# Optimization experiments

Measured on AMD Instinct MI355X. Metric: run time of the kernel, lower is better.

The kernel has to match this reference:

```python
import jax, jax.numpy as jnp
import numpy as np

G = 4          # deformable groups (from offset_and_mask_dim = 3*4*3*3)
K = 9          # 3x3 kernel points
GN_GROUPS = 16 # GroupNorm groups as in DyHead


def conv2d(x, w, stride=1, pad=1, groups=1):
    return jax.lax.conv_general_dilated(
        x, w, (stride, stride), [(pad, pad), (pad, pad)],
        dimension_numbers=('NCHW', 'OIHW', 'NCHW'),
        feature_group_count=groups)


def dw_conv(x, w, scale, bias):
    # YOLO Conv with g=in_channels: depthwise 3x3 + folded BN + SiLU
    C = x.shape[1]
    y = conv2d(x, w, groups=C)
    y = y * scale[None, :, None, None] + bias[None, :, None, None]
    return y * jax.nn.sigmoid(y)


def offset_mask_conv(x, w, b):
    # Conv2d(C, 108, 3, padding=1, groups=4)
    return conv2d(x, w, groups=G) + b[None, :, None, None]


def split_offset_mask(om, use_softmax):
    # om: (N,108,H,W) -> offset (N,H,W,G,K,2) in pixels (dy,dx), mask (N,H,W,G,K)
    N, _, H, W = om.shape
    om = om.transpose(0, 2, 3, 1)
    offset = om[..., :2 * G * K].reshape(N, H, W, G, K, 2)
    m = om[..., 2 * G * K:].reshape(N, H, W, G, K)
    mask = jax.nn.softmax(m, axis=-1) if use_softmax else jax.nn.sigmoid(m)
    return offset, mask


def group_norm(x, gamma, beta, eps=1e-5):
    N, C, H, W = x.shape
    xg = x.reshape(N, GN_GROUPS, C // GN_GROUPS, H, W)
    mu = xg.mean((2, 3, 4), keepdims=True)
    var = xg.var((2, 3, 4), keepdims=True)
    xg = (xg - mu) * jax.lax.rsqrt(var + eps)
    return xg.reshape(N, C, H, W) * gamma[None, :, None, None] + beta[None, :, None, None]


def dcnv3_sample(x, offset, mask, stride):
    # DCNv3 core: group-wise deformable 3x3 bilinear sampling, zero padding.
    # x: (N,C,H,W); offset: (N,Ho,Wo,G,K,2); mask: (N,Ho,Wo,G,K) -> (N,C,Ho,Wo)
    N, C, H, W = x.shape
    Cg = C // G
    Ho, Wo = offset.shape[1], offset.shape[2]
    xg = x.transpose(0, 2, 3, 1).reshape(N, H, W, G, Cg)
    kk = jnp.arange(3, dtype=x.dtype) - 1.0
    ky = jnp.repeat(kk, 3)  # (9,)
    kx = jnp.tile(kk, 3)
    base_y = (jnp.arange(Ho, dtype=x.dtype) * stride)[None, :, None, None, None]
    base_x = (jnp.arange(Wo, dtype=x.dtype) * stride)[None, None, :, None, None]
    py = base_y + ky + offset[..., 0]   # (N,Ho,Wo,G,K)
    px = base_x + kx + offset[..., 1]
    y0 = jnp.floor(py)
    x0 = jnp.floor(px)
    wy = py - y0
    wx = px - x0
    y0i = y0.astype(jnp.int32)
    x0i = x0.astype(jnp.int32)
    n_idx = jnp.arange(N)[:, None, None, None, None]
    g_idx = jnp.arange(G)[None, None, None, :, None]
    acc = jnp.zeros((N, Ho, Wo, G, Cg), x.dtype)
    for dy in (0, 1):
        for dx in (0, 1):
            yi = y0i + dy
            xi = x0i + dx
            w = (wy if dy else 1.0 - wy) * (wx if dx else 1.0 - wx)
            valid = (yi >= 0) & (yi < H) & (xi >= 0) & (xi < W)
            w = w * valid.astype(x.dtype) * mask
            v = xg[n_idx, jnp.clip(yi, 0, H - 1), jnp.clip(xi, 0, W - 1), g_idx]  # (N,Ho,Wo,G,K,Cg)
            acc = acc + jnp.einsum('nhwgk,nhwgkc->nhwgc', w, v)
    return acc.reshape(N, Ho, Wo, C).transpose(0, 3, 1, 2)


def up_bilinear_ac(x, Ho, Wo):
    # bilinear, align_corners=True
    N, C, H, W = x.shape
    def coords(out, size):
        c = jnp.arange(out, dtype=jnp.float32) * ((size - 1) / max(out - 1, 1))
        i0 = jnp.floor(c).astype(jnp.int32)
        i1 = jnp.minimum(i0 + 1, size - 1)
        return i0, i1, (c - i0).astype(x.dtype)
    y0, y1, wy = coords(Ho, H)
    xc0, xc1, wx = coords(Wo, W)
    t = x[:, :, y0, :] * (1.0 - wy)[None, None, :, None] + x[:, :, y1, :] * wy[None, None, :, None]
    return t[:, :, :, xc0] * (1.0 - wx) + t[:, :, :, xc1] * wx


def scale_attn(f, w, b):
    # AdaptiveAvgPool2d(1) -> Conv 1x1 (C->1) -> ReLU -> HSigmoid(bias=3, divisor=6)
    y = f.mean((2, 3))                      # (N,C)
    a = jax.nn.relu(y @ w.T + b)            # (N,1)
    a = jnp.clip((a + 3.0) / 6.0, 0.0, 1.0)
    return f * a[:, :, None, None]


def dyrelu(f, w1, b1_, w2, b2_):
    # DyReLU with K2=True, use_bias=True, lambda_a=2, init_a=[1,0], init_b=[0,0]
    y = f.mean((2, 3))                      # (N,C)
    h = jax.nn.relu(y @ w1.T + b1_)
    z = jnp.clip(h @ w2.T + b2_ + 3.0, 0.0, 6.0) / 6.0  # h_sigmoid
    a1, b1, a2, b2 = jnp.split(z, 4, axis=1)
    a1 = (a1 - 0.5) * 2.0 + 1.0
    a2 = (a2 - 0.5) * 2.0
    b1 = b1 - 0.5
    b2 = b2 - 0.5
    bc = lambda t: t[:, :, None, None]
    return jnp.maximum(f * bc(a1) + bc(b1), f * bc(a2) + bc(b2))


def _forward(x0, x1, x2,
             dw_w_h, dw_s_h, dw_b_h, dw_w_m, dw_s_m, dw_b_m, dw_w_l, dw_s_l, dw_b_l,
             off_w, off_b,
             gn_g_h, gn_b_h, gn_g_m, gn_b_m, gn_g_l, gn_b_l,
             sa_w, sa_b, fc1_w, fc1_b, fc2_w, fc2_b):
    xs = [x0, x1, x2]
    outs = []
    for lvl in range(3):
        x = xs[lvl]
        mid_ = dw_conv(x, dw_w_m, dw_s_m, dw_b_m)
        off, msk = split_offset_mask(offset_mask_conv(mid_, off_w, off_b), use_softmax=False)
        mid_feat = group_norm(dcnv3_sample(x, off, msk, 1), gn_g_m, gn_b_m)
        sum_feat = scale_attn(mid_feat, sa_w, sa_b)
        n_lvls = 1
        if lvl > 0:
            xl = xs[lvl - 1]
            low_ = dw_conv(xl, dw_w_l, dw_s_l, dw_b_l)
            off, msk = split_offset_mask(offset_mask_conv(low_, off_w, off_b), use_softmax=True)
            off = off[:, ::2, ::2]   # stride-2 output grid
            msk = msk[:, ::2, ::2]
            low_feat = group_norm(dcnv3_sample(xl, off, msk, 2), gn_g_l, gn_b_l)
            sum_feat = sum_feat + scale_attn(low_feat, sa_w, sa_b)
            n_lvls += 1
        if lvl < 2:
            xh = xs[lvl + 1]
            high_ = dw_conv(xh, dw_w_h, dw_s_h, dw_b_h)
            off, msk = split_offset_mask(offset_mask_conv(high_, off_w, off_b), use_softmax=True)
            high_feat = group_norm(dcnv3_sample(xh, off, msk, 1), gn_g_h, gn_b_h)
            high_feat = up_bilinear_ac(high_feat, x.shape[2], x.shape[3])
            sum_feat = sum_feat + scale_attn(high_feat, sa_w, sa_b)
            n_lvls += 1
        outs.append(dyrelu(sum_feat / n_lvls, fc1_w, fc1_b, fc2_w, fc2_b))
    return tuple(outs)


def setup_inputs() -> dict:
    key = jax.random.key(0)
    ks = jax.random.split(key, 32)
    N, C = 4, 256
    f32 = jnp.float32
    nrm = lambda k, shape, s=1.0: jax.random.normal(k, shape, f32) * s
    inp = {
        'x0': nrm(ks[0], (N, C, 80, 80)),
        'x1': nrm(ks[1], (N, C, 40, 40)),
        'x2': nrm(ks[2], (N, C, 20, 20)),
        'dw_w_h': nrm(ks[3], (C, 1, 3, 3), 0.1),
        'dw_s_h': 1.0 + nrm(ks[4], (C,), 0.1),
        'dw_b_h': nrm(ks[5], (C,), 0.1),
        'dw_w_m': nrm(ks[6], (C, 1, 3, 3), 0.1),
        'dw_s_m': 1.0 + nrm(ks[7], (C,), 0.1),
        'dw_b_m': nrm(ks[8], (C,), 0.1),
        'dw_w_l': nrm(ks[9], (C, 1, 3, 3), 0.1),
        'dw_s_l': 1.0 + nrm(ks[10], (C,), 0.1),
        'dw_b_l': nrm(ks[11], (C,), 0.1),
        'off_w': nrm(ks[12], (108, C // G, 3, 3), 0.1),
        'off_b': nrm(ks[13], (108,), 0.1),
        'gn_g_h': 1.0 + nrm(ks[14], (C,), 0.1),
        'gn_b_h': nrm(ks[15], (C,), 0.1),
        'gn_g_m': 1.0 + nrm(ks[16], (C,), 0.1),
        'gn_b_m': nrm(ks[17], (C,), 0.1),
        'gn_g_l': 1.0 + nrm(ks[18], (C,), 0.1),
        'gn_b_l': nrm(ks[19], (C,), 0.1),
        'sa_w': nrm(ks[20], (1, C), 0.05),
        'sa_b': nrm(ks[21], (1,), 0.05),
        'fc1_w': nrm(ks[22], (C // 4, C), 0.05),
        'fc1_b': nrm(ks[23], (C // 4,), 0.05),
        'fc2_w': nrm(ks[24], (4 * C, C // 4), 0.05),
        'fc2_b': nrm(ks[25], (4 * C,), 0.1),
    }
    return inp


def reference(x0, x1, x2,
              dw_w_h, dw_s_h, dw_b_h, dw_w_m, dw_s_m, dw_b_m, dw_w_l, dw_s_l, dw_b_l,
              off_w, off_b,
              gn_g_h, gn_b_h, gn_g_m, gn_b_m, gn_g_l, gn_b_l,
              sa_w, sa_b, fc1_w, fc1_b, fc2_w, fc2_b):
    return _forward(x0, x1, x2,
                    dw_w_h, dw_s_h, dw_b_h, dw_w_m, dw_s_m, dw_b_m, dw_w_l, dw_s_l, dw_b_l,
                    off_w, off_b,
                    gn_g_h, gn_b_h, gn_g_m, gn_b_m, gn_g_l, gn_b_l,
                    sa_w, sa_b, fc1_w, fc1_b, fc2_w, fc2_b)
```

## Files before the change

### kernel.cpp

```cpp
#include <hip/hip_runtime.h>
#include <hip/hip_bf16.h>

#define C_ 256
#define G_ 4

typedef __attribute__((ext_vector_type(8))) short bf16x8;
typedef __attribute__((ext_vector_type(4))) float f32x4;

static __device__ __forceinline__ unsigned short f2bf(float x) {
    __hip_bfloat16 h = __float2bfloat16(x);
    return *(unsigned short*)&h;
}
static __device__ __forceinline__ float bf2f(unsigned short u) {
    return __uint_as_float((unsigned)u << 16);
}
static __device__ __forceinline__ float4 bf4(ushort4 u) {
    float4 r;
    r.x = bf2f(u.x);
    r.y = bf2f(u.y);
    r.z = bf2f(u.z);
    r.w = bf2f(u.w);
    return r;
}

__global__ void k_prep(const float* __restrict__ off_w, const float* __restrict__ dwh,
                       const float* __restrict__ dwm, const float* __restrict__ dwl,
                       unsigned short* __restrict__ wmf, float* __restrict__ dwt,
                       float* __restrict__ zeros) {
    int i = blockIdx.x * 256 + threadIdx.x;
    const int NWM = 4 * 32 * 576;
    if (i < NWM) {
        int g = i / (32 * 576), rem = i % (32 * 576);
        int ol = rem / 576, kk = rem % 576;
        int tap = kk / 64, ic = kk % 64;
        float v = (ol < 27) ? off_w[((size_t)((g * 27 + ol) * 64 + ic)) * 9 + tap] : 0.f;
        wmf[i] = f2bf(v);
    }
    int j = i - NWM;
    if (j >= 0 && j < 3 * 2304) {
        int which = j / 2304, rem = j % 2304;
        int t = rem / 256, c = rem % 256;
        const float* src = (which == 0) ? dwh : (which == 1) ? dwm : dwl;
        dwt[j] = src[c * 9 + t];
    }
    int z = i - NWM - 3 * 2304;
    if (z >= 0 && z < 8064) zeros[z] = 0.f;
}

struct TrP {
    const float* x[3];
    unsigned short* xtb[3];
    int H[3];
    int W[3];
    int wtc[3];
    int blk[4];
};

__global__ __launch_bounds__(256) void k_transpose_b(TrP P) {
    __shared__ float tile[32][33];
    int b = blockIdx.x;
    int f = (b >= P.blk[1]) + (b >= P.blk[2]);
    int l = b - P.blk[f];
    int H = P.H[f], W = P.W[f], wtc = P.wtc[f];
    int nh = l / wtc, wtile = l - nh * wtc;
    int n = nh / H, h = nh % H;
    int w0 = wtile * 32, c0 = blockIdx.y * 32;
    const float* x = P.x[f];
    unsigned short* xtb = P.xtb[f];
    int tid = threadIdx.x;
    int i = tid / 32, j = tid % 32;
#pragma unroll
    for (int r = 0; r < 4; r++) {
        int c = c0 + i + r * 8;
        int w = w0 + j;
        tile[i + r * 8][j] = (w < W) ? x[((size_t)(n * C_ + c) * H + h) * W + w] : 0.f;
    }
    __syncthreads();
    int wj = tid >> 4, ci2 = (tid & 15) * 2;
#pragma unroll
    for (int r = 0; r < 2; r++) {
        int w = w0 + wj + r * 16;
        if (w < W) {
            ushort2 o;
            o.x = f2bf(tile[ci2][wj + r * 16]);
            o.y = f2bf(tile[ci2 + 1][wj + r * 16]);
            *(ushort2*)(xtb + ((size_t)(n * H + h) * W + w) * C_ + c0 + ci2) = o;
        }
    }
}

struct DwP {
    const unsigned short* xtb[7];
    unsigned short* out[7];
    const float* wdt[7];
    const float* sc[7];
    const float* bi[7];
    int H[7];
    int W[7];
    int blk[8];
};

__global__ __launch_bounds__(256) void k_dw_silu_b(DwP P) {
    int b = blockIdx.x;
    int f = (b >= P.blk[1]) + (b >= P.blk[2]) + (b >= P.blk[3]) + (b >= P.blk[4]) +
            (b >= P.blk[5]) + (b >= P.blk[6]);
    int H = P.H[f], W = P.W[f];
    const unsigned short* xtbf = P.xtb[f];
    unsigned short* outf = P.out[f];
    const float* wdt = P.wdt[f];
    int tid = threadIdx.x;
    int wv = tid >> 6, lane = tid & 63;
    int half = lane >> 5, l5 = lane & 31;
    int ch8 = l5 << 3;
    int pix = (b - P.blk[f]) * 8 + wv * 2 + half;
    int w = pix % W, h = (pix / W) % H, n = pix / (W * H);
    const float4 sA = *(const float4*)(P.sc[f] + ch8);
    const float4 sB = *(const float4*)(P.sc[f] + ch8 + 4);
    const float4 bA = *(const float4*)(P.bi[f] + ch8);
    const float4 bB = *(const float4*)(P.bi[f] + ch8 + 4);
    const unsigned short* xb = xtbf + (size_t)n * H * W * C_ + ch8;
    float4 accA = {0.f, 0.f, 0.f, 0.f}, accB = {0.f, 0.f, 0.f, 0.f};
#pragma unroll
    for (int t = 0; t < 9; t++) {
        int hh = h + t / 3 - 1, ww = w + t % 3 - 1;
        if (hh >= 0 && hh < H && ww >= 0 && ww < W) {
            bf16x8 xv = *(const bf16x8*)(xb + (size_t)(hh * W + ww) * C_);
            float4 wa = *(const float4*)(wdt + t * 256 + ch8);
            float4 wb = *(const float4*)(wdt + t * 256 + ch8 + 4);
            accA.x += wa.x * bf2f((unsigned short)xv[0]);
            accA.y += wa.y * bf2f((unsigned short)xv[1]);
            accA.z += wa.z * bf2f((unsigned short)xv[2]);
            accA.w += wa.w * bf2f((unsigned short)xv[3]);
            accB.x += wb.x * bf2f((unsigned short)xv[4]);
            accB.y += wb.y * bf2f((unsigned short)xv[5]);
            accB.z += wb.z * bf2f((unsigned short)xv[6]);
            accB.w += wb.w * bf2f((unsigned short)xv[7]);
        }
    }
    float y0 = accA.x * sA.x + bA.x, y1 = accA.y * sA.y + bA.y;
    float y2 = accA.z * sA.z + bA.z, y3 = accA.w * sA.w + bA.w;
    float y4 = accB.x * sB.x + bB.x, y5 = accB.y * sB.y + bB.y;
    float y6 = accB.z * sB.z + bB.z, y7 = accB.w * sB.w + bB.w;
    y0 = y0 / (1.f + __expf(-y0));
    y1 = y1 / (1.f + __expf(-y1));
    y2 = y2 / (1.f + __expf(-y2));
    y3 = y3 / (1.f + __expf(-y3));
    y4 = y4 / (1.f + __expf(-y4));
    y5 = y5 / (1.f + __expf(-y5));
    y6 = y6 / (1.f + __expf(-y6));
    y7 = y7 / (1.f + __expf(-y7));
    uint4 ov;
    ov.x = (unsigned)f2bf(y0) | ((unsigned)f2bf(y1) << 16);
    ov.y = (unsigned)f2bf(y2) | ((unsigned)f2bf(y3) << 16);
    ov.z = (unsigned)f2bf(y4) | ((unsigned)f2bf(y5) << 16);
    ov.w = (unsigned)f2bf(y6) | ((unsigned)f2bf(y7) << 16);
    *(uint4*)(outf + (size_t)pix * C_ + ch8) = ov;
}

struct OmP7 {
    const unsigned short* dwb[7];
    float* om[7];
    int Hs[7], Ws[7], Wo[7], HoWo[7];
    int ss[7];
    int ths[7], tws[7];
    int SR[7], SC[7], Msc[7];
    int nz[7], Mnz[7];
    int blk[8];
};

__global__ __launch_bounds__(256) void k_offmask_b(OmP7 P,
                                                   const unsigned short* __restrict__ wmf) {
    __shared__ __align__(16) char smem[22032];
    unsigned short* patch = (unsigned short*)smem;
    float* omv = (float*)smem;

    int tid = threadIdx.x;
    int wv = tid >> 6, lane = tid & 63;
    int n16 = lane & 15, q = lane >> 4;
    int b = blockIdx.x;
    int f = (b >= P.blk[1]) + (b >= P.blk[2]) + (b >= P.blk[3]) + (b >= P.blk[4]) +
            (b >= P.blk[5]) + (b >= P.blk[6]);
    int l = b - P.blk[f];
    int n = (l >> 2) & 3, g = l & 3;
    int tile = l >> 4;
    int nz = P.nz[f];
    int ty = (tile * P.Mnz[f]) >> 16;
    int tz = tile - ty * nz;
    int ss = P.ss[f], ths = P.ths[f], tws = P.tws[f];
    int TW = 1 << tws;
    int SR = P.SR[f], SC = P.SC[f], Msc = P.Msc[f];
    int NV = SR * SC;
    int Hs = P.Hs[f], Ws = P.Ws[f], Wo = P.Wo[f], HoWo = P.HoWo[f];
    int ho0 = ty << ths, wo0 = tz << tws;
    int hs0 = (ho0 << ss) - 1, ws0 = (wo0 << ss) - 1;
    const unsigned short* dwb = P.dwb[f];
    float* om = P.om[f];

    for (int idx = tid; idx < NV * 8; idx += 256) {
        int pp = idx >> 3;
        int c8 = (idx & 7) << 3;
        int pq = (pp * Msc) >> 16;
        int hh = hs0 + pq, ww = ws0 + (pp - pq * SC);
        uint4 v = {0u, 0u, 0u, 0u};
        if (hh >= 0 && hh < Hs && ww >= 0 && ww < Ws)
            v = *(const uint4*)(dwb + ((size_t)(n * Hs + hh) * Ws + ww) * C_ + g * 64 + c8);
        *(uint4*)(patch + pp * 72 + c8) = v;
    }
    __syncthreads();

    int bchan = q << 3;
    const unsigned short* wg = wmf + (size_t)g * 32 * 576;
    int TP = 1 << (ths + tws);
    int sc1 = SC, sc2 = SC * 2;

    if (TP == 64) {
        int p = wv * 16 + n16;
        int pr = p >> tws, pc = p & (TW - 1);
        int pixbase = (pr << ss) * SC + (pc << ss);
        f32x4 a0 = {0.f, 0.f, 0.f, 0.f}, a1 = {0.f, 0.f, 0.f, 0.f};
#pragma unroll
        for (int kk = 0; kk < 18; kk++) {
            int tap = kk >> 1;
            int ic0 = (kk & 1) << 5;
            int tr = tap / 3, tc = tap % 3;
            int ppix = pixbase + (tr == 0 ? 0 : (tr == 1 ? sc1 : sc2)) + tc;
            bf16x8 bb = *(const bf16x8*)(patch + ppix * 72 + ic0 + bchan);
            bf16x8 wa0 = *(const bf16x8*)(wg + (size_t)n16 * 576 + kk * 32 + bchan);
            bf16x8 wa1 = *(const bf16x8*)(wg + (size_t)(16 + n16) * 576 + kk * 32 + bchan);
            a0 = __builtin_amdgcn_mfma_f32_16x16x32_bf16(wa0, bb, a0, 0, 0, 0);
            a1 = __builtin_amdgcn_mfma_f32_16x16x32_bf16(wa1, bb, a1, 0, 0, 0);
        }
        __syncthreads();
#pragma unroll
        for (int r = 0; r < 4; r++) {
            int ol0 = q * 4 + r;
            omv[p * 28 + ol0] = a0[r];
            int ol1 = 16 + q * 4 + r;
            if (ol1 < 28) omv[p * 28 + ol1] = a1[r];
        }
    } else {
        int NT = TP >> 3;
        int t = wv;
        bool active = t < NT;
        int ntile = t >> 1, mtile = t & 1;
        int p = ntile * 16 + n16;
        int pr = p >> tws, pc = p & (TW - 1);
        int pixbase = (pr << ss) * SC + (pc << ss);
        f32x4 acc = {0.f, 0.f, 0.f, 0.f};
        if (active) {
#pragma unroll
            for (int kk = 0; kk < 18; kk++) {
                int tap = kk >> 1;
                int ic0 = (kk & 1) << 5;
                int tr = tap / 3, tc = tap % 3;
                int ppix = pixbase + (tr == 0 ? 0 : (tr == 1 ? sc1 : sc2)) + tc;
                bf16x8 bb = *(const bf16x8*)(patch + ppix * 72 + ic0 + bchan);
                bf16x8 wa = *(const bf16x8*)(wg + (size_t)(mtile * 16 + n16) * 576 +
                                             kk * 32 + bchan);
                acc = __builtin_amdgcn_mfma_f32_16x16x32_bf16(wa, bb, acc, 0, 0, 0);
            }
        }
        __syncthreads();
        if (active) {
#pragma unroll
            for (int r = 0; r < 4; r++) {
                int ol = mtile * 16 + q * 4 + r;
                if (ol < 28) omv[p * 28 + ol] = acc[r];
            }
        }
    }
    __syncthreads();

    float* omg = om + ((size_t)(g * 4 + n)) * HoWo * 28;
    for (int idx = tid; idx < TP * 7; idx += 256) {
        int p = (idx * 9363) >> 16;
        int c4 = idx - p * 7;
        int ho = ho0 + (p >> tws), wo = wo0 + (p & (TW - 1));
        int pixn = ho * Wo + wo;
        *(float4*)(omg + (size_t)pixn * 28 + c4 * 4) = *(float4*)(omv + p * 28 + c4 * 4);
    }
}

struct SmP {
    const unsigned short* xtb[7];
    const float* om[7];
    float* raw[7];
    float* stats[7];
    int Hs[7];
    int Ws[7];
    int Wo[7];
    int HoWo[7];
    int stride[7];
    int softmax[7];
    int blk[8];
};

__global__ __launch_bounds__(256) void k_sample_b(SmP P, const float* __restrict__ bias) {
    int tid = threadIdx.x;
    int wv = tid >> 6, lane = tid & 63;
    int halfp = lane >> 5, l5 = lane & 31;
    int g = l5 >> 3;
    int ch8 = l5 << 3;
    int nb = gridDim.x;
    int per = nb >> 3, rem = nb & 7;
    int xcd = blockIdx.x & 7, bi = blockIdx.x >> 3;
    int logical = xcd * per + min(xcd, rem) + bi;
    int f = (logical >= P.blk[1]) + (logical >= P.blk[2]) + (logical >= P.blk[3]) +
            (logical >= P.blk[4]) + (logical >= P.blk[5]) + (logical >= P.blk[6]);
    const unsigned short* xtb = P.xtb[f];
    const float* om = P.om[f];
    float* raw = P.raw[f];
    float* stats = P.stats[f];
    int Hs = P.Hs[f], Ws = P.Ws[f], Wo = P.Wo[f], HoWo = P.HoWo[f];
    int stride = P.stride[f], softmax = P.softmax[f];
    int pix0 = (logical - P.blk[f]) * 8;
    int n = pix0 / HoWo;
    int pixn0 = pix0 - n * HoWo;

    __shared__ float lom[8 * 112];
    __shared__ float lb[108];
    __shared__ float sm[32][9];
    __shared__ float4 lw[288];
    __shared__ ushort4 li[288];
    __shared__ float lstat[32];

    if (tid < 224) {
        int gc = tid / 56, r2 = tid % 56;
        int pp = r2 / 7, c4 = r2 % 7;
        float4 v = *(const float4*)(om + ((size_t)(gc * 4 + n) * HoWo + pixn0 + pp) * 28 +
                                    c4 * 4);
        ((float4*)lom)[pp * 28 + gc * 7 + c4] = v;
    }
    if (tid < 108) lb[tid] = bias[tid];
    if (tid < 32) lstat[tid] = 0.f;
    __syncthreads();

    if (tid < 32) {
        int pp = tid >> 2, gs = tid & 3;
        float mv[9];
#pragma unroll
        for (int k = 0; k < 9; k++) {
            int ch = 72 + gs * 9 + k;
            int gc = ch / 27;
            mv[k] = lom[pp * 112 + gc * 28 + (ch - gc * 27)] + lb[ch];
        }
        if (softmax) {
            float mx = -1e30f;
#pragma unroll
            for (int k = 0; k < 9; k++) mx = fmaxf(mx, mv[k]);
            float ssum = 0.f;
#pragma unroll
            for (int k = 0; k < 9; k++) {
                mv[k] = __expf(mv[k] - mx);
                ssum += mv[k];
            }
            float inv = 1.f / ssum;
#pragma unroll
            for (int k = 0; k < 9; k++) sm[tid][k] = mv[k] * inv;
        } else {
#pragma unroll
            for (int k = 0; k < 9; k++) sm[tid][k] = 1.f / (1.f + __expf(-mv[k]));
        }
    }
    __syncthreads();

    for (int idx = tid; idx < 288; idx += 256) {
        int pg = idx / 9, k = idx % 9;
        int pp = pg >> 2, gs = pg & 3;
        int chy = gs * 18 + 2 * k, chx = chy + 1;
        int gcy = chy / 27, gcx = chx / 27;
        float oy = lom[pp * 112 + gcy * 28 + (chy - gcy * 27)] + lb[chy];
        float ox = lom[pp * 112 + gcx * 28 + (chx - gcx * 27)] + lb[chx];
        int pixn = pixn0 + pp;
        int ho = pixn / Wo, wo = pixn % Wo;
        float py = (float)(ho * stride + k / 3 - 1) + oy;
        float px = (float)(wo * stride + k % 3 - 1) + ox;
        float y0f = floorf(py), x0f = floorf(px);
        int y0 = (int)y0f, x0 = (int)x0f;
        float wy = py - y0f, wx = px - x0f;
        int y1 = y0 + 1, x1 = x0 + 1;
        float v0y = (y0 >= 0 && y0 < Hs) ? 1.f : 0.f;
        float v1y = (y1 >= 0 && y1 < Hs) ? 1.f : 0.f;
        float v0x = (x0 >= 0 && x0 < Ws) ? 1.f : 0.f;
        float v1x = (x1 >= 0 && x1 < Ws) ? 1.f : 0.f;
        int y0c = min(max(y0, 0), Hs - 1), y1c = min(max(y1, 0), Hs - 1);
        int x0c = min(max(x0, 0), Ws - 1), x1c = min(max(x1, 0), Ws - 1);
        float m_ = sm[pg][k];
        float4 w4;
        w4.x = (1.f - wy) * (1.f - wx) * v0y * v0x * m_;
        w4.y = (1.f - wy) * wx * v0y * v1x * m_;
        w4.z = wy * (1.f - wx) * v1y * v0x * m_;
        w4.w = wy * wx * v1y * v1x * m_;
        ushort4 i4;
        i4.x = (unsigned short)(y0c * Ws + x0c);
        i4.y = (unsigned short)(y0c * Ws + x1c);
        i4.z = (unsigned short)(y1c * Ws + x0c);
        i4.w = (unsigned short)(y1c * Ws + x1c);
        lw[pp * 36 + gs * 9 + k] = w4;
        li[pp * 36 + gs * 9 + k] = i4;
    }
    __syncthreads();

    int px = wv * 2 + halfp;
    const unsigned short* xb = xtb + (size_t)n * Hs * Ws * C_ + ch8;
    float4 aL = {0.f, 0.f, 0.f, 0.f}, aH = {0.f, 0.f, 0.f, 0.f};
#pragma unroll
    for (int k = 0; k < 9; k++) {
        float4 w4 = lw[px * 36 + g * 9 + k];
        ushort4 i4 = li[px * 36 + g * 9 + k];
        bf16x8 v0 = *(const bf16x8*)(xb + ((size_t)i4.x << 8));
        bf16x8 v1 = *(const bf16x8*)(xb + ((size_t)i4.y << 8));
        bf16x8 v2 = *(const bf16x8*)(xb + ((size_t)i4.z << 8));
        bf16x8 v3 = *(const bf16x8*)(xb + ((size_t)i4.w << 8));
        aL.x += w4.x * bf2f((unsigned short)v0[0]) + w4.y * bf2f((unsigned short)v1[0]) +
                w4.z * bf2f((unsigned short)v2[0]) + w4.w * bf2f((unsigned short)v3[0]);
        aL.y += w4.x * bf2f((unsigned short)v0[1]) + w4.y * bf2f((unsigned short)v1[1]) +
                w4.z * bf2f((unsigned short)v2[1]) + w4.w * bf2f((unsigned short)v3[1]);
        aL.z += w4.x * bf2f((unsigned short)v0[2]) + w4.y * bf2f((unsigned short)v1[2]) +
                w4.z * bf2f((unsigned short)v2[2]) + w4.w * bf2f((unsigned short)v3[2]);
        aL.w += w4.x * bf2f((unsigned short)v0[3]) + w4.y * bf2f((unsigned short)v1[3]) +
                w4.z * bf2f((unsigned short)v2[3]) + w4.w * bf2f((unsigned short)v3[3]);
        aH.x += w4.x * bf2f((unsigned short)v0[4]) + w4.y * bf2f((unsigned short)v1[4]) +
                w4.z * bf2f((unsigned short)v2[4]) + w4.w * bf2f((unsigned short)v3[4]);
        aH.y += w4.x * bf2f((unsigned short)v0[5]) + w4.y * bf2f((unsigned short)v1[5]) +
                w4.z * bf2f((unsigned short)v2[5]) + w4.w * bf2f((unsigned short)v3[5]);
        aH.z += w4.x * bf2f((unsigned short)v0[6]) + w4.y * bf2f((unsigned short)v1[6]) +
                w4.z * bf2f((unsigned short)v2[6]) + w4.w * bf2f((unsigned short)v3[6]);
        aH.w += w4.x * bf2f((unsigned short)v0[7]) + w4.y * bf2f((unsigned short)v1[7]) +
                w4.z * bf2f((unsigned short)v2[7]) + w4.w * bf2f((unsigned short)v3[7]);
    }
    *(float4*)(raw + (size_t)(pix0 + px) * C_ + ch8) = aL;
    *(float4*)(raw + (size_t)(pix0 + px) * C_ + ch8 + 4) = aH;
    float gs = aL.x + aL.y + aL.z + aL.w + aH.x + aH.y + aH.z + aH.w;
    float gss = aL.x * aL.x + aL.y * aL.y + aL.z * aL.z + aL.w * aL.w + aH.x * aH.x +
                aH.y * aH.y + aH.z * aH.z + aH.w * aH.w;
    gs += __shfl_down(gs, 1, 2);
    gss += __shfl_down(gss, 1, 2);
    if ((lane & 1) == 0) {
        atomicAdd(&lstat[(l5 >> 1) * 2 + 0], gs);
        atomicAdd(&lstat[(l5 >> 1) * 2 + 1], gss);
    }
    __syncthreads();
    if (tid < 32) atomicAdd(&stats[n * 32 + tid], lstat[tid]);
}

struct GnP {
    const float* raw[5];
    float* fin[5];
    const float* stats[5];
    float* cmean[5];
    const float* gamma[5];
    const float* beta[5];
    int Hr[5];
    int Wr[5];
    int Hf[5];
    int Wf[5];
    int blk[6];
};

__global__ __launch_bounds__(256) void k_gnup_b(GnP P) {
    int b = blockIdx.x;
    int f = (b >= P.blk[1]) + (b >= P.blk[2]) + (b >= P.blk[3]) + (b >= P.blk[4]);
    int Hr = P.Hr[f], Wr = P.Wr[f], Hf = P.Hf[f], Wf = P.Wf[f];
    const float* raw = P.raw[f];
    float* fin = P.fin[f];
    const float* stats = P.stats[f];
    float* cmean = P.cmean[f];
    int HWf = Hf * Wf;
    int spn = (HWf + 63) >> 6;
    int lb_ = b - P.blk[f];
    int n = lb_ / spn;
    int p0 = (lb_ % spn) << 6;
    int tid = threadIdx.x;
    int wv = tid >> 6, lane = tid & 63;
    int ch4 = lane << 2;
    int gg = lane >> 2;
    float cnt = 16.f * Hr * Wr;
    float s1 = stats[(n * 16 + gg) * 2], s2 = stats[(n * 16 + gg) * 2 + 1];
    float mu = s1 / cnt;
    float var = s2 / cnt - mu * mu;
    float rs = rsqrtf(var + 1e-5f);
    float4 g4 = *(const float4*)(P.gamma[f] + ch4);
    float4 b4 = *(const float4*)(P.beta[f] + ch4);
    float4 ga, be;
    ga.x = g4.x * rs; be.x = b4.x - mu * ga.x;
    ga.y = g4.y * rs; be.y = b4.y - mu * ga.y;
    ga.z = g4.z * rs; be.z = b4.z - mu * ga.z;
    ga.w = g4.w * rs; be.w = b4.w - mu * ga.w;
    bool up = (Hf != Hr);
    float sys = up ? (float)((double)(Hr - 1) / (double)(Hf - 1)) : 0.f;
    float sxs = up ? (float)((double)(Wr - 1) / (double)(Wf - 1)) : 0.f;
    float4 csum = {0.f, 0.f, 0.f, 0.f};
    __shared__ float cs[4][256];
    const float* rb = raw + (size_t)n * Hr * Wr * C_ + ch4;
    for (int i = wv; i < 64; i += 4) {
        int p = p0 + i;
        if (p < HWf) {
            float4 v;
            if (up) {
                int ho = p / Wf, wo = p % Wf;
                float sy = ho * sys, sx = wo * sxs;
                int y0 = (int)sy, x0 = (int)sx;
                float fy = sy - y0, fx = sx - x0;
                int y1 = min(y0 + 1, Hr - 1), x1 = min(x0 + 1, Wr - 1);
                float4 v00 = *(const float4*)(rb + (size_t)(y0 * Wr + x0) * C_);
                float4 v01 = *(const float4*)(rb + (size_t)(y0 * Wr + x1) * C_);
                float4 v10 = *(const float4*)(rb + (size_t)(y1 * Wr + x0) * C_);
                float4 v11 = *(const float4*)(rb + (size_t)(y1 * Wr + x1) * C_);
                v.x = (v00.x * (1.f - fy) + v10.x * fy) * (1.f - fx) + (v01.x * (1.f - fy) + v11.x * fy) * fx;
                v.y = (v00.y * (1.f - fy) + v10.y * fy) * (1.f - fx) + (v01.y * (1.f - fy) + v11.y * fy) * fx;
                v.z = (v00.z * (1.f - fy) + v10.z * fy) * (1.f - fx) + (v01.z * (1.f - fy) + v11.z * fy) * fx;
                v.w = (v00.w * (1.f - fy) + v10.w * fy) * (1.f - fx) + (v01.w * (1.f - fy) + v11.w * fy) * fx;
            } else {
                v = *(const float4*)(raw + ((size_t)n * HWf + p) * C_ + ch4);
            }
            float4 y4;
            y4.x = v.x * ga.x + be.x;
            y4.y = v.y * ga.y + be.y;
            y4.z = v.z * ga.z + be.z;
            y4.w = v.w * ga.w + be.w;
            *(float4*)(fin + ((size_t)n * HWf + p) * C_ + ch4) = y4;
            csum.x += y4.x; csum.y += y4.y; csum.z += y4.z; csum.w += y4.w;
        }
    }
    cs[wv][ch4 + 0] = csum.x;
    cs[wv][ch4 + 1] = csum.y;
    cs[wv][ch4 + 2] = csum.z;
    cs[wv][ch4 + 3] = csum.w;
    __syncthreads();
    if (wv == 0) {
        float t0 = 0.f, t1 = 0.f, t2 = 0.f, t3 = 0.f;
#pragma unroll
        for (int r = 0; r < 4; r++) {
            t0 += cs[r][ch4 + 0];
            t1 += cs[r][ch4 + 1];
            t2 += cs[r][ch4 + 2];
            t3 += cs[r][ch4 + 3];
        }
        atomicAdd(&cmean[n * C_ + ch4 + 0], t0);
        atomicAdd(&cmean[n * C_ + ch4 + 1], t1);
        atomicAdd(&cmean[n * C_ + ch4 + 2], t2);
        atomicAdd(&cmean[n * C_ + ch4 + 3], t3);
    }
}

struct CfP {
    int nf[3];
    float inv_nl[3];
    float inv_hw[3];
    int slot[3];
};

__global__ __launch_bounds__(256) void k_coef_b(CfP P, const float* __restrict__ cmean_base,
                                                const float* __restrict__ sa_w,
                                                const float* __restrict__ sa_b,
                                                const float* __restrict__ fc1_w,
                                                const float* __restrict__ fc1_b,
                                                const float* __restrict__ fc2_w,
                                                const float* __restrict__ fc2_b,
                                                float* __restrict__ coef,
                                                float* __restrict__ af) {
    int lvl = blockIdx.x >> 2;
    int n = blockIdx.x & 3;
    int nf = P.nf[lvl];
    float inv_nl = P.inv_nl[lvl], inv_hw = P.inv_hw[lvl];
    int slot = P.slot[lvl];
    int c = threadIdx.x;
    __shared__ float red[256];
    __shared__ float meanv[256];
    __shared__ float hv[64];
    __shared__ float sa_a[3];
    float cm[3] = {0.f, 0.f, 0.f};
    for (int f = 0; f < nf; f++) {
        cm[f] = cmean_base[(size_t)(slot + f) * 1024 + n * C_ + c] * inv_hw;
        red[c] = sa_w[c] * cm[f];
        __syncthreads();
        for (int s = 128; s; s >>= 1) {
            if (c < s) red[c] += red[c + s];
            __syncthreads();
        }
        if (c == 0) {
            float t = fmaxf(red[0] + sa_b[0], 0.f);
            sa_a[f] = fminf(fmaxf((t + 3.f) * (1.f / 6.f), 0.f), 1.f);
        }
        __syncthreads();
    }
    float mv = 0.f;
    for (int f = 0; f < nf; f++) mv += sa_a[f] * cm[f];
    mv *= inv_nl;
    meanv[c] = mv;
    __syncthreads();
    int j = c >> 2, t = c & 3;
    float partial = 0.f;
    for (int k = t * 64; k < t * 64 + 64; k++) partial += fc1_w[j * 256 + k] * meanv[k];
    partial += __shfl_down(partial, 2, 4);
    partial += __shfl_down(partial, 1, 4);
    if (t == 0) hv[j] = fmaxf(partial + fc1_b[j], 0.f);
    __syncthreads();
    float zz[4];
#pragma unroll
    for (int i = 0; i < 4; i++) {
        float z = fc2_b[i * 256 + c];
        for (int k = 0; k < 64; k++) z += fc2_w[(size_t)(i * 256 + c) * 64 + k] * hv[k];
        zz[i] = fminf(fmaxf(z + 3.f, 0.f), 6.f) * (1.f / 6.f);
    }
    float* cf = coef + lvl * 4096;
    cf[n * 1024 + 0 * 256 + c] = (zz[0] - 0.5f) * 2.f + 1.f;
    cf[n * 1024 + 1 * 256 + c] = zz[1] - 0.5f;
    cf[n * 1024 + 2 * 256 + c] = (zz[2] - 0.5f) * 2.f;
    cf[n * 1024 + 3 * 256 + c] = zz[3] - 0.5f;
    if (c < 4) af[lvl * 16 + n * 4 + c] = (c < nf) ? sa_a[c] * inv_nl : 0.f;
}

struct StP {
    const float* fA[3];
    const float* fB[3];
    const float* fC[3];
    float* out[3];
    int nf[3];
    int HW[3];
    int npt[3];
    int blk[4];
};

__global__ __launch_bounds__(256) void k_store_b(StP P, const float* __restrict__ coef,
                                                 const float* __restrict__ af) {
    __shared__ float tile[64][65];
    int b = blockIdx.x;
    int f = (b >= P.blk[1]) + (b >= P.blk[2]);
    int l = b - P.blk[f];
    int npt = P.npt[f], HW = P.HW[f], nf = P.nf[f];
    int n = l / (npt * 4);
    int r_ = l - n * (npt * 4);
    int pt = r_ >> 2;
    int c0 = (r_ & 3) * 64;
    const float* fA = P.fA[f];
    const float* fB = P.fB[f];
    const float* fC = P.fC[f];
    float* out = P.out[f];
    const float* coefL = coef + f * 4096;
    const float* afL = af + f * 16;
    int tid = threadIdx.x;
    int lane16 = tid & 15, prow = tid >> 4;
    int ch4 = c0 + lane16 * 4;
    float a0 = afL[n * 4 + 0], a1f = afL[n * 4 + 1], a2f = afL[n * 4 + 2];
    float4 ca1 = *(const float4*)(coefL + n * 1024 + 0 + ch4);
    float4 cb1 = *(const float4*)(coefL + n * 1024 + 256 + ch4);
    float4 ca2 = *(const float4*)(coefL + n * 1024 + 512 + ch4);
    float4 cb2 = *(const float4*)(coefL + n * 1024 + 768 + ch4);
#pragma unroll
    for (int pass = 0; pass < 4; pass++) {
        int px = pass * 16 + prow;
        int p = pt * 64 + px;
        if (p < HW) {
            size_t base = ((size_t)n * HW + p) * C_ + ch4;
            float4 v = *(const float4*)(fA + base);
            float4 fv;
            fv.x = v.x * a0;
            fv.y = v.y * a0;
            fv.z = v.z * a0;
            fv.w = v.w * a0;
            if (nf > 1) {
                float4 vb = *(const float4*)(fB + base);
                fv.x += vb.x * a1f;
                fv.y += vb.y * a1f;
                fv.z += vb.z * a1f;
                fv.w += vb.w * a1f;
            }
            if (nf > 2) {
                float4 vc = *(const float4*)(fC + base);
                fv.x += vc.x * a2f;
                fv.y += vc.y * a2f;
                fv.z += vc.z * a2f;
                fv.w += vc.w * a2f;
            }
            int cr = lane16 * 4;
            tile[cr + 0][px] = fmaxf(fv.x * ca1.x + cb1.x, fv.x * ca2.x + cb2.x);
            tile[cr + 1][px] = fmaxf(fv.y * ca1.y + cb1.y, fv.y * ca2.y + cb2.y);
            tile[cr + 2][px] = fmaxf(fv.z * ca1.z + cb1.z, fv.z * ca2.z + cb2.z);
            tile[cr + 3][px] = fmaxf(fv.w * ca1.w + cb1.w, fv.w * ca2.w + cb2.w);
        }
    }
    __syncthreads();
#pragma unroll
    for (int wp = 0; wp < 4; wp++) {
        int row = wp * 16 + (tid >> 4);
        int px4 = (tid & 15) * 4;
        int p = pt * 64 + px4;
        if (p < HW) {
            float4 r;
            r.x = tile[row][px4 + 0];
            r.y = tile[row][px4 + 1];
            r.z = tile[row][px4 + 2];
            r.w = tile[row][px4 + 3];
            *(float4*)(out + (size_t)(n * C_ + c0 + row) * HW + p) = r;
        }
    }
}

extern "C" void kernel_launch(void* const* d_in, const int* in_sizes, int n_in,
                              void* d_out, int out_size, void* d_ws, size_t ws_size,
                              hipStream_t stream) {
    (void)in_sizes; (void)n_in; (void)out_size; (void)ws_size;
    const float* x0 = (const float*)d_in[0];
    const float* x1 = (const float*)d_in[1];
    const float* x2 = (const float*)d_in[2];
    const float* dw_w_h = (const float*)d_in[3];
    const float* dw_s_h = (const float*)d_in[4];
    const float* dw_b_h = (const float*)d_in[5];
    const float* dw_w_m = (const float*)d_in[6];
    const float* dw_s_m = (const float*)d_in[7];
    const float* dw_b_m = (const float*)d_in[8];
    const float* dw_w_l = (const float*)d_in[9];
    const float* dw_s_l = (const float*)d_in[10];
    const float* dw_b_l = (const float*)d_in[11];
    const float* off_w = (const float*)d_in[12];
    const float* off_b = (const float*)d_in[13];
    const float* gn_g_h = (const float*)d_in[14];
    const float* gn_b_h = (const float*)d_in[15];
    const float* gn_g_m = (const float*)d_in[16];
    const float* gn_b_m = (const float*)d_in[17];
    const float* gn_g_l = (const float*)d_in[18];
    const float* gn_b_l = (const float*)d_in[19];
    const float* sa_w = (const float*)d_in[20];
    const float* sa_b = (const float*)d_in[21];
    const float* fc1_w = (const float*)d_in[22];
    const float* fc1_b = (const float*)d_in[23];
    const float* fc2_w = (const float*)d_in[24];
    const float* fc2_b = (const float*)d_in[25];

    float* ws = (float*)d_ws;
    unsigned short* XTB0 = (unsigned short*)(ws + 0);
    unsigned short* XTB1 = (unsigned short*)(ws + 3276800);
    unsigned short* XTB2 = (unsigned short*)(ws + 4096000);
    float* XTBF = ws;
    float* SH = ws + 4300800;
    float* FINA = ws + 10854400;
    float* FINB = ws + 17408000;
    float* FINC = ws + 23961600;
    float* WMF = ws + 25600000;
    float* DWT = ws + 25636864;
    float* STATS = ws + 25643776;
    float* CMEAN = ws + 25644672;

    unsigned short* SHB = (unsigned short*)SH;
    unsigned short* FINAB = (unsigned short*)FINA;
    unsigned short* WMFB = (unsigned short*)WMF;

    float* out0 = (float*)d_out;
    float* out1 = out0 + 6553600;
    float* out2 = out0 + 8192000;

    float* OM_l0mid = out0;
    float* OM_l0high = out0 + 2867200;
    float* OM_l1mid = out0 + 3584000;
    float* OM_l1low = out0 + 4300800;
    float* OM_l1high = out1;
    float* OM_l2mid = out1 + 179200;
    float* OM_l2low = out1 + 358400;

    float* RAW_l0mid = SH;
    float* RAW_l0high = FINC;
    float* RAW_l1mid = FINB;
    float* RAW_l1low = FINB + 1638400;
    float* RAW_l1high = FINB + 3276800;
    float* RAW_l2mid = FINB + 3686400;
    float* RAW_l2low = FINB + 4096000;
    float* FIN_l0mid = FINA;
    float* FIN_l0high = FINB;
    float* FIN_l1mid = XTBF;
    float* FIN_l1low = XTBF + 1638400;
    float* FIN_l1high = SH;
    float* FIN_l2mid = XTBF + 3276800;
    float* FIN_l2low = XTBF + 3686400;
    float* COEF = FINC;
    float* AF = FINC + 12288;

    k_prep<<<(4 * 32 * 576 + 6912 + 8064 + 255) / 256, 256, 0, stream>>>(
        off_w, dw_w_h, dw_w_m, dw_w_l, WMFB, DWT, STATS);

    {
        TrP tp{};
        tp.x[0] = x0; tp.xtb[0] = XTB0; tp.H[0] = 80; tp.W[0] = 80; tp.wtc[0] = 3;
        tp.x[1] = x1; tp.xtb[1] = XTB1; tp.H[1] = 40; tp.W[1] = 40; tp.wtc[1] = 2;
        tp.x[2] = x2; tp.xtb[2] = XTB2; tp.H[2] = 20; tp.W[2] = 20; tp.wtc[2] = 1;
        tp.blk[0] = 0; tp.blk[1] = 960; tp.blk[2] = 1280; tp.blk[3] = 1360;
        k_transpose_b<<<dim3(1360, 8), 256, 0, stream>>>(tp);
    }

    unsigned short* DWB_x0mid = SHB;
    unsigned short* DWB_x0low = SHB + 6553600;
    unsigned short* DWB_x1high = FINAB;
    unsigned short* DWB_x1mid = FINAB + 1638400;
    unsigned short* DWB_x1low = FINAB + 3276800;
    unsigned short* DWB_x2high = FINAB + 4915200;
    unsigned short* DWB_x2mid = FINAB + 5324800;

    {
        DwP dp{};
        dp.xtb[0] = XTB0; dp.out[0] = DWB_x0mid;  dp.wdt[0] = DWT + 1 * 2304;
        dp.sc[0] = dw_s_m; dp.bi[0] = dw_b_m; dp.H[0] = 80; dp.W[0] = 80;
        dp.xtb[1] = XTB0; dp.out[1] = DWB_x0low;  dp.wdt[1] = DWT + 2 * 2304;
        dp.sc[1] = dw_s_l; dp.bi[1] = dw_b_l; dp.H[1] = 80; dp.W[1] = 80;
        dp.xtb[2] = XTB1; dp.out[2] = DWB_x1high; dp.wdt[2] = DWT + 0 * 2304;
        dp.sc[2] = dw_s_h; dp.bi[2] = dw_b_h; dp.H[2] = 40; dp.W[2] = 40;
        dp.xtb[3] = XTB1; dp.out[3] = DWB_x1mid;  dp.wdt[3] = DWT + 1 * 2304;
        dp.sc[3] = dw_s_m; dp.bi[3] = dw_b_m; dp.H[3] = 40; dp.W[3] = 40;
        dp.xtb[4] = XTB1; dp.out[4] = DWB_x1low;  dp.wdt[4] = DWT + 2 * 2304;
        dp.sc[4] = dw_s_l; dp.bi[4] = dw_b_l; dp.H[4] = 40; dp.W[4] = 40;
        dp.xtb[5] = XTB2; dp.out[5] = DWB_x2high; dp.wdt[5] = DWT + 0 * 2304;
        dp.sc[5] = dw_s_h; dp.bi[5] = dw_b_h; dp.H[5] = 20; dp.W[5] = 20;
        dp.xtb[6] = XTB2; dp.out[6] = DWB_x2mid;  dp.wdt[6] = DWT + 1 * 2304;
        dp.sc[6] = dw_s_m; dp.bi[6] = dw_b_m; dp.H[6] = 20; dp.W[6] = 20;
        dp.blk[0] = 0;    dp.blk[1] = 3200; dp.blk[2] = 6400; dp.blk[3] = 7200;
        dp.blk[4] = 8000; dp.blk[5] = 8800; dp.blk[6] = 9000; dp.blk[7] = 9200;
        k_dw_silu_b<<<9200, 256, 0, stream>>>(dp);
    }

    {
        OmP7 op{};
        auto setf = [&](int i, const unsigned short* dwb, float* om, int Hs, int Ws,
                        int Wo, int HoWo, int ss, int ths, int tws, int SR, int SC,
                        int nz) {
            op.dwb[i] = dwb; op.om[i] = om;
            op.Hs[i] = Hs; op.Ws[i] = Ws; op.Wo[i] = Wo; op.HoWo[i] = HoWo;
            op.ss[i] = ss; op.ths[i] = ths; op.tws[i] = tws;
            op.SR[i] = SR; op.SC[i] = SC; op.Msc[i] = (65536 + SC - 1) / SC;
            op.nz[i] = nz; op.Mnz[i] = (65536 + nz - 1) / nz;
        };
        setf(0, DWB_x0mid,  OM_l0mid,  80, 80, 80, 6400, 0, 3, 3, 10, 10, 10);
        setf(1, DWB_x1high, OM_l0high, 40, 40, 40, 1600, 0, 2, 3, 6,  10, 5);
        setf(2, DWB_x1mid,  OM_l1mid,  40, 40, 40, 1600, 0, 2, 3, 6,  10, 5);
        setf(3, DWB_x0low,  OM_l1low,  80, 80, 40, 1600, 1, 2, 3, 9,  17, 5);
        setf(4, DWB_x2high, OM_l1high, 20, 20, 20, 400,  0, 2, 2, 6,  6,  5);
        setf(5, DWB_x2mid,  OM_l2mid,  20, 20, 20, 400,  0, 2, 2, 6,  6,  5);
        setf(6, DWB_x1low,  OM_l2low,  40, 40, 20, 400,  1, 2, 2, 9,  9,  5);
        op.blk[0] = 0;    op.blk[1] = 1600; op.blk[2] = 2400; op.blk[3] = 3200;
        op.blk[4] = 4000; op.blk[5] = 4400; op.blk[6] = 4800; op.blk[7] = 5200;
        k_offmask_b<<<5200, 256, 0, stream>>>(op, WMFB);
    }

    {
        SmP sp{};
        sp.xtb[0] = XTB0; sp.om[0] = OM_l0mid;  sp.raw[0] = RAW_l0mid;  sp.stats[0] = STATS + 0 * 128;
        sp.Hs[0] = 80; sp.Ws[0] = 80; sp.Wo[0] = 80; sp.HoWo[0] = 6400; sp.stride[0] = 1; sp.softmax[0] = 0;
        sp.xtb[1] = XTB1; sp.om[1] = OM_l0high; sp.raw[1] = RAW_l0high; sp.stats[1] = STATS + 1 * 128;
        sp.Hs[1] = 40; sp.Ws[1] = 40; sp.Wo[1] = 40; sp.HoWo[1] = 1600; sp.stride[1] = 1; sp.softmax[1] = 1;
        sp.xtb[2] = XTB1; sp.om[2] = OM_l1mid;  sp.raw[2] = RAW_l1mid;  sp.stats[2] = STATS + 2 * 128;
        sp.Hs[2] = 40; sp.Ws[2] = 40; sp.Wo[2] = 40; sp.HoWo[2] = 1600; sp.stride[2] = 1; sp.softmax[2] = 0;
        sp.xtb[3] = XTB0; sp.om[3] = OM_l1low;  sp.raw[3] = RAW_l1low;  sp.stats[3] = STATS + 3 * 128;
        sp.Hs[3] = 80; sp.Ws[3] = 80; sp.Wo[3] = 40; sp.HoWo[3] = 1600; sp.stride[3] = 2; sp.softmax[3] = 1;
        sp.xtb[4] = XTB2; sp.om[4] = OM_l1high; sp.raw[4] = RAW_l1high; sp.stats[4] = STATS + 4 * 128;
        sp.Hs[4] = 20; sp.Ws[4] = 20; sp.Wo[4] = 20; sp.HoWo[4] = 400;  sp.stride[4] = 1; sp.softmax[4] = 1;
        sp.xtb[5] = XTB2; sp.om[5] = OM_l2mid;  sp.raw[5] = RAW_l2mid;  sp.stats[5] = STATS + 5 * 128;
        sp.Hs[5] = 20; sp.Ws[5] = 20; sp.Wo[5] = 20; sp.HoWo[5] = 400;  sp.stride[5] = 1; sp.softmax[5] = 0;
        sp.xtb[6] = XTB1; sp.om[6] = OM_l2low;  sp.raw[6] = RAW_l2low;  sp.stats[6] = STATS + 6 * 128;
        sp.Hs[6] = 40; sp.Ws[6] = 40; sp.Wo[6] = 20; sp.HoWo[6] = 400;  sp.stride[6] = 2; sp.softmax[6] = 1;
        sp.blk[0] = 0;    sp.blk[1] = 3200; sp.blk[2] = 4000; sp.blk[3] = 4800;
        sp.blk[4] = 5600; sp.blk[5] = 5800; sp.blk[6] = 6000; sp.blk[7] = 6200;
        k_sample_b<<<6200, 256, 0, stream>>>(sp, off_b);
    }

    {
        GnP gp{};
        gp.raw[0] = RAW_l0mid; gp.fin[0] = FIN_l0mid; gp.stats[0] = STATS + 0 * 128;
        gp.cmean[0] = CMEAN + 0 * 1024; gp.gamma[0] = gn_g_m; gp.beta[0] = gn_b_m;
        gp.Hr[0] = 80; gp.Wr[0] = 80; gp.Hf[0] = 80; gp.Wf[0] = 80;
        gp.blk[0] = 0; gp.blk[1] = 400; gp.blk[2] = 400;
        gp.blk[3] = 400; gp.blk[4] = 400; gp.blk[5] = 400;
        k_gnup_b<<<400, 256, 0, stream>>>(gp);
    }
    {
        GnP gp{};
        gp.raw[0] = RAW_l1mid;  gp.fin[0] = FIN_l1mid;  gp.stats[0] = STATS + 2 * 128;
        gp.cmean[0] = CMEAN + 2 * 1024; gp.gamma[0] = gn_g_m; gp.beta[0] = gn_b_m;
        gp.Hr[0] = 40; gp.Wr[0] = 40; gp.Hf[0] = 40; gp.Wf[0] = 40;
        gp.raw[1] = RAW_l1low;  gp.fin[1] = FIN_l1low;  gp.stats[1] = STATS + 3 * 128;
        gp.cmean[1] = CMEAN + 3 * 1024; gp.gamma[1] = gn_g_l; gp.beta[1] = gn_b_l;
        gp.Hr[1] = 40; gp.Wr[1] = 40; gp.Hf[1] = 40; gp.Wf[1] = 40;
        gp.raw[2] = RAW_l1high; gp.fin[2] = FIN_l1high; gp.stats[2] = STATS + 4 * 128;
        gp.cmean[2] = CMEAN + 4 * 1024; gp.gamma[2] = gn_g_h; gp.beta[2] = gn_b_h;
        gp.Hr[2] = 20; gp.Wr[2] = 20; gp.Hf[2] = 40; gp.Wf[2] = 40;
        gp.raw[3] = RAW_l2mid;  gp.fin[3] = FIN_l2mid;  gp.stats[3] = STATS + 5 * 128;
        gp.cmean[3] = CMEAN + 5 * 1024; gp.gamma[3] = gn_g_m; gp.beta[3] = gn_b_m;
        gp.Hr[3] = 20; gp.Wr[3] = 20; gp.Hf[3] = 20; gp.Wf[3] = 20;
        gp.raw[4] = RAW_l2low;  gp.fin[4] = FIN_l2low;  gp.stats[4] = STATS + 6 * 128;
        gp.cmean[4] = CMEAN + 6 * 1024; gp.gamma[4] = gn_g_l; gp.beta[4] = gn_b_l;
        gp.Hr[4] = 20; gp.Wr[4] = 20; gp.Hf[4] = 20; gp.Wf[4] = 20;
        gp.blk[0] = 0; gp.blk[1] = 100; gp.blk[2] = 200;
        gp.blk[3] = 300; gp.blk[4] = 328; gp.blk[5] = 356;
        k_gnup_b<<<356, 256, 0, stream>>>(gp);
    }
    {
        GnP gp{};
        gp.raw[0] = RAW_l0high; gp.fin[0] = FIN_l0high; gp.stats[0] = STATS + 1 * 128;
        gp.cmean[0] = CMEAN + 1 * 1024; gp.gamma[0] = gn_g_h; gp.beta[0] = gn_b_h;
        gp.Hr[0] = 40; gp.Wr[0] = 40; gp.Hf[0] = 80; gp.Wf[0] = 80;
        gp.blk[0] = 0; gp.blk[1] = 400; gp.blk[2] = 400;
        gp.blk[3] = 400; gp.blk[4] = 400; gp.blk[5] = 400;
        k_gnup_b<<<400, 256, 0, stream>>>(gp);
    }

    {
        CfP cp{};
        cp.nf[0] = 2; cp.inv_nl[0] = 0.5f;       cp.inv_hw[0] = 1.f / 6400.f; cp.slot[0] = 0;
        cp.nf[1] = 3; cp.inv_nl[1] = 1.f / 3.f;  cp.inv_hw[1] = 1.f / 1600.f; cp.slot[1] = 2;
        cp.nf[2] = 2; cp.inv_nl[2] = 0.5f;       cp.inv_hw[2] = 1.f / 400.f;  cp.slot[2] = 5;
        k_coef_b<<<12, 256, 0, stream>>>(cp, CMEAN, sa_w, sa_b, fc1_w, fc1_b, fc2_w, fc2_b,
                                         COEF, AF);
    }

    {
        StP st{};
        st.fA[0] = FIN_l0mid; st.fB[0] = FIN_l0high; st.fC[0] = nullptr; st.out[0] = out0;
        st.nf[0] = 2; st.HW[0] = 6400; st.npt[0] = 100;
        st.fA[1] = FIN_l1mid; st.fB[1] = FIN_l1low;  st.fC[1] = FIN_l1high; st.out[1] = out1;
        st.nf[1] = 3; st.HW[1] = 1600; st.npt[1] = 25;
        st.fA[2] = FIN_l2mid; st.fB[2] = FIN_l2low;  st.fC[2] = nullptr; st.out[2] = out2;
        st.nf[2] = 2; st.HW[2] = 400;  st.npt[2] = 7;
        st.blk[0] = 0; st.blk[1] = 1600; st.blk[2] = 2000; st.blk[3] = 2112;
        k_store_b<<<2112, 256, 0, stream>>>(st, COEF, AF);
    }
}
```

Before: 405.6 us.

## Eliminate GroupNorm/upsample pass by folding into sampler and store kernels

```diff
diff --git a/kernel.cpp b/kernel.cpp
--- a/kernel.cpp
+++ b/kernel.cpp
@@ -14,13 +14,21 @@
 static __device__ __forceinline__ float bf2f(unsigned short u) {
     return __uint_as_float((unsigned)u << 16);
 }
-static __device__ __forceinline__ float4 bf4(ushort4 u) {
-    float4 r;
-    r.x = bf2f(u.x);
-    r.y = bf2f(u.y);
-    r.z = bf2f(u.z);
-    r.w = bf2f(u.w);
-    return r;
+
+static __device__ __forceinline__ float upw(int y, int Hr, int Hf, float sys) {
+    float inv = 1.f / sys;
+    int lo = max(0, (int)((y - 1) * inv) - 1);
+    int hi = min(Hf - 1, (int)((y + 1) * inv) + 1);
+    float w = 0.f;
+    for (int o = lo; o <= hi; o++) {
+        float sy = o * sys;
+        int y0 = (int)sy;
+        float fy = sy - y0;
+        int y1 = min(y0 + 1, Hr - 1);
+        if (y0 == y) w += 1.f - fy;
+        if (y1 == y) w += fy;
+    }
+    return w;
 }
 
 __global__ void k_prep(const float* __restrict__ off_w, const float* __restrict__ dwh,
@@ -286,12 +294,18 @@
     const float* om[7];
     float* raw[7];
     float* stats[7];
+    float* rsum[7];
     int Hs[7];
     int Ws[7];
     int Wo[7];
     int HoWo[7];
     int stride[7];
     int softmax[7];
+    int up[7];
+    int Hf[7];
+    int Wf2[7];
+    float sys[7];
+    float sxs[7];
     int blk[8];
 };
 
@@ -311,8 +325,10 @@
     const float* om = P.om[f];
     float* raw = P.raw[f];
     float* stats = P.stats[f];
+    float* rsum = P.rsum[f];
     int Hs = P.Hs[f], Ws = P.Ws[f], Wo = P.Wo[f], HoWo = P.HoWo[f];
     int stride = P.stride[f], softmax = P.softmax[f];
+    int upf = P.up[f];
     int pix0 = (logical - P.blk[f]) * 8;
     int n = pix0 / HoWo;
     int pixn0 = pix0 - n * HoWo;
@@ -323,6 +339,8 @@
     __shared__ float4 lw[288];
     __shared__ ushort4 li[288];
     __shared__ float lstat[32];
+    __shared__ float lsum[8][256];
+    __shared__ float wup[8];
 
     if (tid < 224) {
         int gc = tid / 56, r2 = tid % 56;
@@ -361,6 +379,16 @@
 #pragma unroll
             for (int k = 0; k < 9; k++) sm[tid][k] = 1.f / (1.f + __expf(-mv[k]));
         }
+    }
+    if (tid < 8) {
+        float w = 1.f;
+        if (upf) {
+            int Ho = HoWo / Wo;
+            int pixn = pixn0 + tid;
+            int ho = pixn / Wo, wo = pixn - ho * Wo;
+            w = upw(ho, Ho, P.Hf[f], P.sys[f]) * upw(wo, Wo, P.Wf2[f], P.sxs[f]);
+        }
+        wup[tid] = w;
     }
     __syncthreads();
 
@@ -431,6 +459,8 @@
     }
     *(float4*)(raw + (size_t)(pix0 + px) * C_ + ch8) = aL;
     *(float4*)(raw + (size_t)(pix0 + px) * C_ + ch8 + 4) = aH;
+    *(float4*)&lsum[px][ch8] = aL;
+    *(float4*)&lsum[px][ch8 + 4] = aH;
     float gs = aL.x + aL.y + aL.z + aL.w + aH.x + aH.y + aH.z + aH.w;
     float gss = aL.x * aL.x + aL.y * aL.y + aL.z * aL.z + aL.w * aL.w + aH.x * aH.x +
                 aH.y * aH.y + aH.z * aH.z + aH.w * aH.w;
@@ -442,116 +472,29 @@
     }
     __syncthreads();
     if (tid < 32) atomicAdd(&stats[n * 32 + tid], lstat[tid]);
-}
-
-struct GnP {
-    const float* raw[5];
-    float* fin[5];
-    const float* stats[5];
-    float* cmean[5];
-    const float* gamma[5];
-    const float* beta[5];
-    int Hr[5];
-    int Wr[5];
-    int Hf[5];
-    int Wf[5];
-    int blk[6];
+    {
+        float s = 0.f;
+#pragma unroll
+        for (int p2 = 0; p2 < 8; p2++) s += wup[p2] * lsum[p2][tid];
+        atomicAdd(&rsum[n * 256 + tid], s);
+    }
+}
+
+struct CfF {
+    const float* rsum;
+    const float* stats;
+    const float* gamma;
+    const float* beta;
+    float cnt;
 };
-
-__global__ __launch_bounds__(256) void k_gnup_b(GnP P) {
-    int b = blockIdx.x;
-    int f = (b >= P.blk[1]) + (b >= P.blk[2]) + (b >= P.blk[3]) + (b >= P.blk[4]);
-    int Hr = P.Hr[f], Wr = P.Wr[f], Hf = P.Hf[f], Wf = P.Wf[f];
-    const float* raw = P.raw[f];
-    float* fin = P.fin[f];
-    const float* stats = P.stats[f];
-    float* cmean = P.cmean[f];
-    int HWf = Hf * Wf;
-    int spn = (HWf + 63) >> 6;
-    int lb_ = b - P.blk[f];
-    int n = lb_ / spn;
-    int p0 = (lb_ % spn) << 6;
-    int tid = threadIdx.x;
-    int wv = tid >> 6, lane = tid & 63;
-    int ch4 = lane << 2;
-    int gg = lane >> 2;
-    float cnt = 16.f * Hr * Wr;
-    float s1 = stats[(n * 16 + gg) * 2], s2 = stats[(n * 16 + gg) * 2 + 1];
-    float mu = s1 / cnt;
-    float var = s2 / cnt - mu * mu;
-    float rs = rsqrtf(var + 1e-5f);
-    float4 g4 = *(const float4*)(P.gamma[f] + ch4);
-    float4 b4 = *(const float4*)(P.beta[f] + ch4);
-    float4 ga, be;
-    ga.x = g4.x * rs; be.x = b4.x - mu * ga.x;
-    ga.y = g4.y * rs; be.y = b4.y - mu * ga.y;
-    ga.z = g4.z * rs; be.z = b4.z - mu * ga.z;
-    ga.w = g4.w * rs; be.w = b4.w - mu * ga.w;
-    bool up = (Hf != Hr);
-    float sys = up ? (float)((double)(Hr - 1) / (double)(Hf - 1)) : 0.f;
-    float sxs = up ? (float)((double)(Wr - 1) / (double)(Wf - 1)) : 0.f;
-    float4 csum = {0.f, 0.f, 0.f, 0.f};
-    __shared__ float cs[4][256];
-    const float* rb = raw + (size_t)n * Hr * Wr * C_ + ch4;
-    for (int i = wv; i < 64; i += 4) {
-        int p = p0 + i;
-        if (p < HWf) {
-            float4 v;
-            if (up) {
-                int ho = p / Wf, wo = p % Wf;
-                float sy = ho * sys, sx = wo * sxs;
-                int y0 = (int)sy, x0 = (int)sx;
-                float fy = sy - y0, fx = sx - x0;
-                int y1 = min(y0 + 1, Hr - 1), x1 = min(x0 + 1, Wr - 1);
-                float4 v00 = *(const float4*)(rb + (size_t)(y0 * Wr + x0) * C_);
-                float4 v01 = *(const float4*)(rb + (size_t)(y0 * Wr + x1) * C_);
-                float4 v10 = *(const float4*)(rb + (size_t)(y1 * Wr + x0) * C_);
-                float4 v11 = *(const float4*)(rb + (size_t)(y1 * Wr + x1) * C_);
-                v.x = (v00.x * (1.f - fy) + v10.x * fy) * (1.f - fx) + (v01.x * (1.f - fy) + v11.x * fy) * fx;
-                v.y = (v00.y * (1.f - fy) + v10.y * fy) * (1.f - fx) + (v01.y * (1.f - fy) + v11.y * fy) * fx;
-                v.z = (v00.z * (1.f - fy) + v10.z * fy) * (1.f - fx) + (v01.z * (1.f - fy) + v11.z * fy) * fx;
-                v.w = (v00.w * (1.f - fy) + v10.w * fy) * (1.f - fx) + (v01.w * (1.f - fy) + v11.w * fy) * fx;
-            } else {
-                v = *(const float4*)(raw + ((size_t)n * HWf + p) * C_ + ch4);
-            }
-            float4 y4;
-            y4.x = v.x * ga.x + be.x;
-            y4.y = v.y * ga.y + be.y;
-            y4.z = v.z * ga.z + be.z;
-            y4.w = v.w * ga.w + be.w;
-            *(float4*)(fin + ((size_t)n * HWf + p) * C_ + ch4) = y4;
-            csum.x += y4.x; csum.y += y4.y; csum.z += y4.z; csum.w += y4.w;
-        }
-    }
-    cs[wv][ch4 + 0] = csum.x;
-    cs[wv][ch4 + 1] = csum.y;
-    cs[wv][ch4 + 2] = csum.z;
-    cs[wv][ch4 + 3] = csum.w;
-    __syncthreads();
-    if (wv == 0) {
-        float t0 = 0.f, t1 = 0.f, t2 = 0.f, t3 = 0.f;
-#pragma unroll
-        for (int r = 0; r < 4; r++) {
-            t0 += cs[r][ch4 + 0];
-            t1 += cs[r][ch4 + 1];
-            t2 += cs[r][ch4 + 2];
-            t3 += cs[r][ch4 + 3];
-        }
-        atomicAdd(&cmean[n * C_ + ch4 + 0], t0);
-        atomicAdd(&cmean[n * C_ + ch4 + 1], t1);
-        atomicAdd(&cmean[n * C_ + ch4 + 2], t2);
-        atomicAdd(&cmean[n * C_ + ch4 + 3], t3);
-    }
-}
-
 struct CfP {
+    CfF ft[3][3];
     int nf[3];
     float inv_nl[3];
     float inv_hw[3];
-    int slot[3];
 };
 
-__global__ __launch_bounds__(256) void k_coef_b(CfP P, const float* __restrict__ cmean_base,
+__global__ __launch_bounds__(256) void k_coef_b(CfP P,
                                                 const float* __restrict__ sa_w,
                                                 const float* __restrict__ sa_b,
                                                 const float* __restrict__ fc1_w,
@@ -564,19 +507,26 @@
     int n = blockIdx.x & 3;
     int nf = P.nf[lvl];
     float inv_nl = P.inv_nl[lvl], inv_hw = P.inv_hw[lvl];
-    int slot = P.slot[lvl];
     int c = threadIdx.x;
     __shared__ float red[256];
     __shared__ float meanv[256];
     __shared__ float hv[64];
     __shared__ float sa_a[3];
     float cm[3] = {0.f, 0.f, 0.f};
+    int gg = c >> 4;
     for (int f = 0; f < nf; f++) {
-        cm[f] = cmean_base[(size_t)(slot + f) * 1024 + n * C_ + c] * inv_hw;
+        CfF s = P.ft[lvl][f];
+        float s1 = s.stats[(n * 16 + gg) * 2], s2 = s.stats[(n * 16 + gg) * 2 + 1];
+        float mu = s1 / s.cnt;
+        float var = s2 / s.cnt - mu * mu;
+        float rs = rsqrtf(var + 1e-5f);
+        float ga = s.gamma[c] * rs;
+        float be = s.beta[c] - mu * ga;
+        cm[f] = ga * s.rsum[n * 256 + c] * inv_hw + be;
         red[c] = sa_w[c] * cm[f];
         __syncthreads();
-        for (int s = 128; s; s >>= 1) {
-            if (c < s) red[c] += red[c + s];
+        for (int st = 128; st; st >>= 1) {
+            if (c < st) red[c] += red[c + st];
             __syncthreads();
         }
         if (c == 0) {
@@ -612,13 +562,24 @@
     if (c < 4) af[lvl * 16 + n * 4 + c] = (c < nf) ? sa_a[c] * inv_nl : 0.f;
 }
 
+struct StF {
+    const float* raw;
+    const float* stats;
+    const float* gamma;
+    const float* beta;
+    float cnt;
+    int up;
+    int Hr;
+    int Wr;
+    float sys;
+    float sxs;
+};
 struct StP {
-    const float* fA[3];
-    const float* fB[3];
-    const float* fC[3];
+    StF ft[3][3];
     float* out[3];
     int nf[3];
     int HW[3];
+    int Wf[3];
     int npt[3];
     int blk[4];
 };
@@ -629,50 +590,84 @@
     int b = blockIdx.x;
     int f = (b >= P.blk[1]) + (b >= P.blk[2]);
     int l = b - P.blk[f];
-    int npt = P.npt[f], HW = P.HW[f], nf = P.nf[f];
+    int npt = P.npt[f], HW = P.HW[f], Wf = P.Wf[f], nf = P.nf[f];
     int n = l / (npt * 4);
     int r_ = l - n * (npt * 4);
     int pt = r_ >> 2;
     int c0 = (r_ & 3) * 64;
-    const float* fA = P.fA[f];
-    const float* fB = P.fB[f];
-    const float* fC = P.fC[f];
     float* out = P.out[f];
     const float* coefL = coef + f * 4096;
     const float* afL = af + f * 16;
     int tid = threadIdx.x;
     int lane16 = tid & 15, prow = tid >> 4;
     int ch4 = c0 + lane16 * 4;
+    int gg = ch4 >> 4;
     float a0 = afL[n * 4 + 0], a1f = afL[n * 4 + 1], a2f = afL[n * 4 + 2];
     float4 ca1 = *(const float4*)(coefL + n * 1024 + 0 + ch4);
     float4 cb1 = *(const float4*)(coefL + n * 1024 + 256 + ch4);
     float4 ca2 = *(const float4*)(coefL + n * 1024 + 512 + ch4);
     float4 cb2 = *(const float4*)(coefL + n * 1024 + 768 + ch4);
+
+    StF sA = P.ft[f][0], sB = P.ft[f][1], sC = P.ft[f][2];
+    auto mkgb = [&](const StF& s, float4& ga, float4& be) {
+        float s1 = s.stats[(n * 16 + gg) * 2], s2 = s.stats[(n * 16 + gg) * 2 + 1];
+        float mu = s1 / s.cnt;
+        float var = s2 / s.cnt - mu * mu;
+        float rs = rsqrtf(var + 1e-5f);
+        float4 gm = *(const float4*)(s.gamma + ch4);
+        float4 bt = *(const float4*)(s.beta + ch4);
+        ga.x = gm.x * rs; be.x = bt.x - mu * ga.x;
+        ga.y = gm.y * rs; be.y = bt.y - mu * ga.y;
+        ga.z = gm.z * rs; be.z = bt.z - mu * ga.z;
+        ga.w = gm.w * rs; be.w = bt.w - mu * ga.w;
+    };
+    float4 gaA, beA, gaB, beB, gaC = {0, 0, 0, 0}, beC = {0, 0, 0, 0};
+    mkgb(sA, gaA, beA);
+    mkgb(sB, gaB, beB);
+    if (nf > 2) mkgb(sC, gaC, beC);
+
+    auto rdf = [&](const StF& s, int p) -> float4 {
+        if (!s.up) return *(const float4*)(s.raw + ((size_t)n * HW + p) * C_ + ch4);
+        int ho = p / Wf, wo = p - ho * Wf;
+        float sy = ho * s.sys, sx = wo * s.sxs;
+        int y0 = (int)sy, x0 = (int)sx;
+        float fy = sy - y0, fx = sx - x0;
+        int y1 = min(y0 + 1, s.Hr - 1), x1 = min(x0 + 1, s.Wr - 1);
+        const float* rb = s.raw + (size_t)n * s.Hr * s.Wr * C_ + ch4;
+        float4 v00 = *(const float4*)(rb + (size_t)(y0 * s.Wr + x0) * C_);
+        float4 v01 = *(const float4*)(rb + (size_t)(y0 * s.Wr + x1) * C_);
+        float4 v10 = *(const float4*)(rb + (size_t)(y1 * s.Wr + x0) * C_);
+        float4 v11 = *(const float4*)(rb + (size_t)(y1 * s.Wr + x1) * C_);
+        float4 v;
+        v.x = (v00.x * (1.f - fy) + v10.x * fy) * (1.f - fx) + (v01.x * (1.f - fy) + v11.x * fy) * fx;
+        v.y = (v00.y * (1.f - fy) + v10.y * fy) * (1.f - fx) + (v01.y * (1.f - fy) + v11.y * fy) * fx;
+        v.z = (v00.z * (1.f - fy) + v10.z * fy) * (1.f - fx) + (v01.z * (1.f - fy) + v11.z * fy) * fx;
+        v.w = (v00.w * (1.f - fy) + v10.w * fy) * (1.f - fx) + (v01.w * (1.f - fy) + v11.w * fy) * fx;
+        return v;
+    };
+
 #pragma unroll
     for (int pass = 0; pass < 4; pass++) {
         int px = pass * 16 + prow;
         int p = pt * 64 + px;
         if (p < HW) {
-            size_t base = ((size_t)n * HW + p) * C_ + ch4;
-            float4 v = *(const float4*)(fA + base);
+            float4 vA = rdf(sA, p);
             float4 fv;
-            fv.x = v.x * a0;
-            fv.y = v.y * a0;
-            fv.z = v.z * a0;
-            fv.w = v.w * a0;
-            if (nf > 1) {
-                float4 vb = *(const float4*)(fB + base);
-                fv.x += vb.x * a1f;
-                fv.y += vb.y * a1f;
-                fv.z += vb.z * a1f;
-                fv.w += vb.w * a1f;
-            }
+            fv.x = (vA.x * gaA.x + beA.x) * a0;
+            fv.y = (vA.y * gaA.y + beA.y) * a0;
+            fv.z = (vA.z * gaA.z + beA.z) * a0;
+            fv.w = (vA.w * gaA.w + beA.w) * a0;
+            float4 vB = rdf(sB, p);
+            fv.x += (vB.x * gaB.x + beB.x) * a1f;
+            fv.y += (vB.y * gaB.y + beB.y) * a1f;
+            fv.z += (vB.z * gaB.z + beB.z) * a1f;
+            fv.w += (vB.w * gaB.w + beB.w) * a1f;
             if (nf > 2) {
-                float4 vc = *(const float4*)(fC + base);
-                fv.x += vc.x * a2f;
-                fv.y += vc.y * a2f;
-                fv.z += vc.z * a2f;
-                fv.w += vc.w * a2f;
+                float4 vC = rdf(sC, p);
+                fv.x += (vC.x * gaC.x + beC.x) * a2f;
+                fv.y += (vC.y * gaC.y + beC.y) * a2f;
+                fv.z += (vC.z * gaC.z + beC.z) * a2f;
+                fv.w += (vC.w * gaC.w + beC.w) * a2f;
             }
             int cr = lane16 * 4;
             tile[cr + 0][px] = fmaxf(fv.x * ca1.x + cb1.x, fv.x * ca2.x + cb2.x);
@@ -733,7 +728,6 @@
     unsigned short* XTB0 = (unsigned short*)(ws + 0);
     unsigned short* XTB1 = (unsigned short*)(ws + 3276800);
     unsigned short* XTB2 = (unsigned short*)(ws + 4096000);
-    float* XTBF = ws;
     float* SH = ws + 4300800;
     float* FINA = ws + 10854400;
     float* FINB = ws + 17408000;
@@ -741,7 +735,7 @@
     float* WMF = ws + 25600000;
     float* DWT = ws + 25636864;
     float* STATS = ws + 25643776;
-    float* CMEAN = ws + 25644672;
+    float* RAWSUM = ws + 25644672;
 
     unsigned short* SHB = (unsigned short*)SH;
     unsigned short* FINAB = (unsigned short*)FINA;
@@ -766,15 +760,11 @@
     float* RAW_l1high = FINB + 3276800;
     float* RAW_l2mid = FINB + 3686400;
     float* RAW_l2low = FINB + 4096000;
-    float* FIN_l0mid = FINA;
-    float* FIN_l0high = FINB;
-    float* FIN_l1mid = XTBF;
-    float* FIN_l1low = XTBF + 1638400;
-    float* FIN_l1high = SH;
-    float* FIN_l2mid = XTBF + 3276800;
-    float* FIN_l2low = XTBF + 3686400;
-    float* COEF = FINC;
-    float* AF = FINC + 12288;
+    float* COEF = FINA;
+    float* AF = FINA + 12288;
+
+    const float SYS_L0H = (float)(39.0 / 79.0);
+    const float SYS_L1H = (float)(19.0 / 39.0);
 
     k_prep<<<(4 * 32 * 576 + 6912 + 8064 + 255) / 256, 256, 0, stream>>>(
         off_w, dw_w_h, dw_w_m, dw_w_l, WMFB, DWT, STATS);
@@ -842,82 +832,57 @@
 
     {
         SmP sp{};
-        sp.xtb[0] = XTB0; sp.om[0] = OM_l0mid;  sp.raw[0] = RAW_l0mid;  sp.stats[0] = STATS + 0 * 128;
-        sp.Hs[0] = 80; sp.Ws[0] = 80; sp.Wo[0] = 80; sp.HoWo[0] = 6400; sp.stride[0] = 1; sp.softmax[0] = 0;
-        sp.xtb[1] = XTB1; sp.om[1] = OM_l0high; sp.raw[1] = RAW_l0high; sp.stats[1] = STATS + 1 * 128;
-        sp.Hs[1] = 40; sp.Ws[1] = 40; sp.Wo[1] = 40; sp.HoWo[1] = 1600; sp.stride[1] = 1; sp.softmax[1] = 1;
-        sp.xtb[2] = XTB1; sp.om[2] = OM_l1mid;  sp.raw[2] = RAW_l1mid;  sp.stats[2] = STATS + 2 * 128;
-        sp.Hs[2] = 40; sp.Ws[2] = 40; sp.Wo[2] = 40; sp.HoWo[2] = 1600; sp.stride[2] = 1; sp.softmax[2] = 0;
-        sp.xtb[3] = XTB0; sp.om[3] = OM_l1low;  sp.raw[3] = RAW_l1low;  sp.stats[3] = STATS + 3 * 128;
-        sp.Hs[3] = 80; sp.Ws[3] = 80; sp.Wo[3] = 40; sp.HoWo[3] = 1600; sp.stride[3] = 2; sp.softmax[3] = 1;
-        sp.xtb[4] = XTB2; sp.om[4] = OM_l1high; sp.raw[4] = RAW_l1high; sp.stats[4] = STATS + 4 * 128;
-        sp.Hs[4] = 20; sp.Ws[4] = 20; sp.Wo[4] = 20; sp.HoWo[4] = 400;  sp.stride[4] = 1; sp.softmax[4] = 1;
-        sp.xtb[5] = XTB2; sp.om[5] = OM_l2mid;  sp.raw[5] = RAW_l2mid;  sp.stats[5] = STATS + 5 * 128;
-        sp.Hs[5] = 20; sp.Ws[5] = 20; sp.Wo[5] = 20; sp.HoWo[5] = 400;  sp.stride[5] = 1; sp.softmax[5] = 0;
-        sp.xtb[6] = XTB1; sp.om[6] = OM_l2low;  sp.raw[6] = RAW_l2low;  sp.stats[6] = STATS + 6 * 128;
-        sp.Hs[6] = 40; sp.Ws[6] = 40; sp.Wo[6] = 20; sp.HoWo[6] = 400;  sp.stride[6] = 2; sp.softmax[6] = 1;
+        auto setf = [&](int i, const unsigned short* xtb, const float* om, float* raw,
+                        int slot, int Hs, int Ws, int Wo, int HoWo, int stride,
+                        int softmax, int up, int Hf, int Wf2, float sys, float sxs) {
+            sp.xtb[i] = xtb; sp.om[i] = om; sp.raw[i] = raw;
+            sp.stats[i] = STATS + slot * 128;
+            sp.rsum[i] = RAWSUM + slot * 1024;
+            sp.Hs[i] = Hs; sp.Ws[i] = Ws; sp.Wo[i] = Wo; sp.HoWo[i] = HoWo;
+            sp.stride[i] = stride; sp.softmax[i] = softmax;
+            sp.up[i] = up; sp.Hf[i] = Hf; sp.Wf2[i] = Wf2;
+            sp.sys[i] = sys; sp.sxs[i] = sxs;
+        };
+        setf(0, XTB0, OM_l0mid,  RAW_l0mid,  0, 80, 80, 80, 6400, 1, 0, 0, 80, 80, 1.f, 1.f);
+        setf(1, XTB1, OM_l0high, RAW_l0high, 1, 40, 40, 40, 1600, 1, 1, 1, 80, 80, SYS_L0H, SYS_L0H);
+        setf(2, XTB1, OM_l1mid,  RAW_l1mid,  2, 40, 40, 40, 1600, 1, 0, 0, 40, 40, 1.f, 1.f);
+        setf(3, XTB0, OM_l1low,  RAW_l1low,  3, 80, 80, 40, 1600, 2, 1, 0, 40, 40, 1.f, 1.f);
+        setf(4, XTB2, OM_l1high, RAW_l1high, 4, 20, 20, 20, 400,  1, 1, 1, 40, 40, SYS_L1H, SYS_L1H);
+        setf(5, XTB2, OM_l2mid,  RAW_l2mid,  5, 20, 20, 20, 400,  1, 0, 0, 20, 20, 1.f, 1.f);
+        setf(6, XTB1, OM_l2low,  RAW_l2low,  6, 40, 40, 20, 400,  2, 1, 0, 20, 20, 1.f, 1.f);
         sp.blk[0] = 0;    sp.blk[1] = 3200; sp.blk[2] = 4000; sp.blk[3] = 4800;
         sp.blk[4] = 5600; sp.blk[5] = 5800; sp.blk[6] = 6000; sp.blk[7] = 6200;
         k_sample_b<<<6200, 256, 0, stream>>>(sp, off_b);
     }
 
     {
-        GnP gp{};
-        gp.raw[0] = RAW_l0mid; gp.fin[0] = FIN_l0mid; gp.stats[0] = STATS + 0 * 128;
-        gp.cmean[0] = CMEAN + 0 * 1024; gp.gamma[0] = gn_g_m; gp.beta[0] = gn_b_m;
-        gp.Hr[0] = 80; gp.Wr[0] = 80; gp.Hf[0] = 80; gp.Wf[0] = 80;
-        gp.blk[0] = 0; gp.blk[1] = 400; gp.blk[2] = 400;
-        gp.blk[3] = 400; gp.blk[4] = 400; gp.blk[5] = 400;
-        k_gnup_b<<<400, 256, 0, stream>>>(gp);
-    }
-    {
-        GnP gp{};
-        gp.raw[0] = RAW_l1mid;  gp.fin[0] = FIN_l1mid;  gp.stats[0] = STATS + 2 * 128;
-        gp.cmean[0] = CMEAN + 2 * 1024; gp.gamma[0] = gn_g_m; gp.beta[0] = gn_b_m;
-        gp.Hr[0] = 40; gp.Wr[0] = 40; gp.Hf[0] = 40; gp.Wf[0] = 40;
-        gp.raw[1] = RAW_l1low;  gp.fin[1] = FIN_l1low;  gp.stats[1] = STATS + 3 * 128;
-        gp.cmean[1] = CMEAN + 3 * 1024; gp.gamma[1] = gn_g_l; gp.beta[1] = gn_b_l;
-        gp.Hr[1] = 40; gp.Wr[1] = 40; gp.Hf[1] = 40; gp.Wf[1] = 40;
-        gp.raw[2] = RAW_l1high; gp.fin[2] = FIN_l1high; gp.stats[2] = STATS + 4 * 128;
-        gp.cmean[2] = CMEAN + 4 * 1024; gp.gamma[2] = gn_g_h; gp.beta[2] = gn_b_h;
-        gp.Hr[2] = 20; gp.Wr[2] = 20; gp.Hf[2] = 40; gp.Wf[2] = 40;
-        gp.raw[3] = RAW_l2mid;  gp.fin[3] = FIN_l2mid;  gp.stats[3] = STATS + 5 * 128;
-        gp.cmean[3] = CMEAN + 5 * 1024; gp.gamma[3] = gn_g_m; gp.beta[3] = gn_b_m;
-        gp.Hr[3] = 20; gp.Wr[3] = 20; gp.Hf[3] = 20; gp.Wf[3] = 20;
-        gp.raw[4] = RAW_l2low;  gp.fin[4] = FIN_l2low;  gp.stats[4] = STATS + 6 * 128;
-        gp.cmean[4] = CMEAN + 6 * 1024; gp.gamma[4] = gn_g_l; gp.beta[4] = gn_b_l;
-        gp.Hr[4] = 20; gp.Wr[4] = 20; gp.Hf[4] = 20; gp.Wf[4] = 20;
-        gp.blk[0] = 0; gp.blk[1] = 100; gp.blk[2] = 200;
-        gp.blk[3] = 300; gp.blk[4] = 328; gp.blk[5] = 356;
-        k_gnup_b<<<356, 256, 0, stream>>>(gp);
-    }
-    {
-        GnP gp{};
-        gp.raw[0] = RAW_l0high; gp.fin[0] = FIN_l0high; gp.stats[0] = STATS + 1 * 128;
-        gp.cmean[0] = CMEAN + 1 * 1024; gp.gamma[0] = gn_g_h; gp.beta[0] = gn_b_h;
-        gp.Hr[0] = 40; gp.Wr[0] = 40; gp.Hf[0] = 80; gp.Wf[0] = 80;
-        gp.blk[0] = 0; gp.blk[1] = 400; gp.blk[2] = 400;
-        gp.blk[3] = 400; gp.blk[4] = 400; gp.blk[5] = 400;
-        k_gnup_b<<<400, 256, 0, stream>>>(gp);
-    }
-
-    {
         CfP cp{};
-        cp.nf[0] = 2; cp.inv_nl[0] = 0.5f;       cp.inv_hw[0] = 1.f / 6400.f; cp.slot[0] = 0;
-        cp.nf[1] = 3; cp.inv_nl[1] = 1.f / 3.f;  cp.inv_hw[1] = 1.f / 1600.f; cp.slot[1] = 2;
-        cp.nf[2] = 2; cp.inv_nl[2] = 0.5f;       cp.inv_hw[2] = 1.f / 400.f;  cp.slot[2] = 5;
-        k_coef_b<<<12, 256, 0, stream>>>(cp, CMEAN, sa_w, sa_b, fc1_w, fc1_b, fc2_w, fc2_b,
+        cp.nf[0] = 2; cp.inv_nl[0] = 0.5f;      cp.inv_hw[0] = 1.f / 6400.f;
+        cp.nf[1] = 3; cp.inv_nl[1] = 1.f / 3.f; cp.inv_hw[1] = 1.f / 1600.f;
+        cp.nf[2] = 2; cp.inv_nl[2] = 0.5f;      cp.inv_hw[2] = 1.f / 400.f;
+        cp.ft[0][0] = {RAWSUM + 0 * 1024, STATS + 0 * 128, gn_g_m, gn_b_m, 102400.f};
+        cp.ft[0][1] = {RAWSUM + 1 * 1024, STATS + 1 * 128, gn_g_h, gn_b_h, 25600.f};
+        cp.ft[1][0] = {RAWSUM + 2 * 1024, STATS + 2 * 128, gn_g_m, gn_b_m, 25600.f};
+        cp.ft[1][1] = {RAWSUM + 3 * 1024, STATS + 3 * 128, gn_g_l, gn_b_l, 25600.f};
+        cp.ft[1][2] = {RAWSUM + 4 * 1024, STATS + 4 * 128, gn_g_h, gn_b_h, 6400.f};
+        cp.ft[2][0] = {RAWSUM + 5 * 1024, STATS + 5 * 128, gn_g_m, gn_b_m, 6400.f};
+        cp.ft[2][1] = {RAWSUM + 6 * 1024, STATS + 6 * 128, gn_g_l, gn_b_l, 6400.f};
+        k_coef_b<<<12, 256, 0, stream>>>(cp, sa_w, sa_b, fc1_w, fc1_b, fc2_w, fc2_b,
                                          COEF, AF);
     }
 
     {
         StP st{};
-        st.fA[0] = FIN_l0mid; st.fB[0] = FIN_l0high; st.fC[0] = nullptr; st.out[0] = out0;
-        st.nf[0] = 2; st.HW[0] = 6400; st.npt[0] = 100;
-        st.fA[1] = FIN_l1mid; st.fB[1] = FIN_l1low;  st.fC[1] = FIN_l1high; st.out[1] = out1;
-        st.nf[1] = 3; st.HW[1] = 1600; st.npt[1] = 25;
-        st.fA[2] = FIN_l2mid; st.fB[2] = FIN_l2low;  st.fC[2] = nullptr; st.out[2] = out2;
-        st.nf[2] = 2; st.HW[2] = 400;  st.npt[2] = 7;
+        st.out[0] = out0; st.nf[0] = 2; st.HW[0] = 6400; st.Wf[0] = 80; st.npt[0] = 100;
+        st.out[1] = out1; st.nf[1] = 3; st.HW[1] = 1600; st.Wf[1] = 40; st.npt[1] = 25;
+        st.out[2] = out2; st.nf[2] = 2; st.HW[2] = 400;  st.Wf[2] = 20; st.npt[2] = 7;
+        st.ft[0][0] = {RAW_l0mid,  STATS + 0 * 128, gn_g_m, gn_b_m, 102400.f, 0, 80, 80, 1.f, 1.f};
+        st.ft[0][1] = {RAW_l0high, STATS + 1 * 128, gn_g_h, gn_b_h, 25600.f,  1, 40, 40, SYS_L0H, SYS_L0H};
+        st.ft[1][0] = {RAW_l1mid,  STATS + 2 * 128, gn_g_m, gn_b_m, 25600.f,  0, 40, 40, 1.f, 1.f};
+        st.ft[1][1] = {RAW_l1low,  STATS + 3 * 128, gn_g_l, gn_b_l, 25600.f,  0, 40, 40, 1.f, 1.f};
+        st.ft[1][2] = {RAW_l1high, STATS + 4 * 128, gn_g_h, gn_b_h, 6400.f,   1, 20, 20, SYS_L1H, SYS_L1H};
+        st.ft[2][0] = {RAW_l2mid,  STATS + 5 * 128, gn_g_m, gn_b_m, 6400.f,   0, 20, 20, 1.f, 1.f};
+        st.ft[2][1] = {RAW_l2low,  STATS + 6 * 128, gn_g_l, gn_b_l, 6400.f,   0, 20, 20, 1.f, 1.f};
         st.blk[0] = 0; st.blk[1] = 1600; st.blk[2] = 2000; st.blk[3] = 2112;
         k_store_b<<<2112, 256, 0, stream>>>(st, COEF, AF);
     }
```

After: 357.6 us. 11.8% less time.
